# Optimization experiments

Hardware: AMD Instinct MI355X
Metric: run time of the kernel (lower is better)

## Reference

```python
import jax, jax.numpy as jnp
import numpy as np

DIM = 1024
DIM_HEAD = 64
HEADS = 8
INNER = DIM_HEAD * HEADS
EPS = 1e-5


def setup_inputs() -> dict:
    key = jax.random.key(0)
    ks = jax.random.split(key, 5)
    b, n = 4, 2048
    x = jax.random.normal(ks[0], (b, n, DIM), dtype=jnp.float32)
    mask = jnp.ones((b, n), dtype=bool)
    gamma = jnp.ones((DIM,), dtype=jnp.float32)
    null_kv = jax.random.normal(ks[1], (HEADS, 2, DIM_HEAD), dtype=jnp.float32)
    w_qkv = jax.random.normal(ks[2], (DIM, INNER * 3), dtype=jnp.float32) * (DIM ** -0.5)
    w_out = jax.random.normal(ks[3], (INNER, DIM), dtype=jnp.float32) * (INNER ** -0.5)
    return {"x": x, "mask": mask, "gamma": gamma, "null_kv": null_kv,
            "w_qkv": w_qkv, "w_out": w_out}


def _attention(x, mask, gamma, null_kv, w_qkv, w_out):
    b, n, _ = x.shape
    scale = DIM_HEAD ** -0.5
    # RMSNorm (sum-based, as in source): x * rsqrt(sum(x^2) + eps) * gamma * sqrt(dim)
    inv = jax.lax.rsqrt(jnp.sum(x * x, axis=-1, keepdims=True) + EPS)
    xn = x * inv * gamma * (DIM ** 0.5)
    qkv = xn @ w_qkv  # [b, n, 3*inner]
    q, k, v = jnp.split(qkv, 3, axis=-1)
    # b n (h d) -> b h n d
    to_heads = lambda t: t.reshape(b, n, HEADS, DIM_HEAD).transpose(0, 2, 1, 3)
    q, k, v = to_heads(q), to_heads(k), to_heads(v)
    # null kv token prepended along the key axis
    nk = jnp.broadcast_to(null_kv[:, 0][None, :, None, :], (b, HEADS, 1, DIM_HEAD))
    nv = jnp.broadcast_to(null_kv[:, 1][None, :, None, :], (b, HEADS, 1, DIM_HEAD))
    k = jnp.concatenate([nk, k], axis=2)  # [b, h, n+1, d]
    v = jnp.concatenate([nv, v], axis=2)
    q = q * scale
    sim = jnp.einsum('bhid,bhjd->bhij', q, k)  # [b, h, n, n+1]
    max_neg = -jnp.finfo(sim.dtype).max
    # padding mask, padded with True for the null token
    pad_mask = jnp.concatenate([jnp.ones((b, 1), dtype=bool), mask], axis=1)  # [b, n+1]
    sim = jnp.where(pad_mask[:, None, None, :], sim, max_neg)
    # causal mask over the non-null keys; null token (j=0) always visible
    j_idx = jnp.arange(n + 1)
    i_idx = jnp.arange(n)
    causal = (j_idx[None, :] - 1) > i_idx[:, None]  # True where masked
    sim = jnp.where(causal[None, None, :, :], max_neg, sim)
    attn = jax.nn.softmax(sim, axis=-1)
    out = jnp.einsum('bhij,bhjd->bhid', attn, v)  # [b, h, n, d]
    out = out.transpose(0, 2, 1, 3).reshape(b, n, INNER)
    return out @ w_out


def reference(x, mask, gamma, null_kv, w_qkv, w_out):
    return _attention(x, mask, gamma, null_kv, w_qkv, w_out)
```

## Files before the change

### kernel.cpp

```cpp
#include <hip/hip_runtime.h>

typedef unsigned short ushort_t;
typedef __attribute__((ext_vector_type(8))) unsigned short u16x8;
typedef __attribute__((ext_vector_type(4))) unsigned short u16x4;
typedef __attribute__((ext_vector_type(8))) __bf16 bf16x8;
typedef __attribute__((ext_vector_type(4))) float f32x4;

#define NB 4
#define NSEQ 2048
#define NH 8
#define DH 64
#define DMODEL 1024
#define INNERD 512

__device__ inline float b2f(unsigned short s) {
  union { unsigned u; float f; } v; v.u = ((unsigned)s) << 16; return v.f;
}
__device__ inline unsigned short f2b(float f) {
  unsigned u = __float_as_uint(f);
  u += 0x7fffu + ((u >> 16) & 1u);
  return (unsigned short)(u >> 16);
}
__device__ inline float fexp2(float x) {
  float r; asm("v_exp_f32 %0, %1" : "=v"(r) : "v"(x)); return r;
}
__device__ inline f32x4 mfma16(u16x8 a, u16x8 b, f32x4 c) {
  return __builtin_amdgcn_mfma_f32_16x16x32_bf16(
      __builtin_bit_cast(bf16x8, a), __builtin_bit_cast(bf16x8, b), c, 0, 0, 0);
}
__device__ inline void gload_lds16(const ushort_t* g, ushort_t* l) {
  __builtin_amdgcn_global_load_lds(
      (const __attribute__((address_space(1))) void*)g,
      (__attribute__((address_space(3))) void*)l, 16, 0, 0);
}

__global__ __launch_bounds__(256) void transconv_k(const float* __restrict__ in,
                                                   ushort_t* __restrict__ out,
                                                   int R, int C) {
  __shared__ float t[32][33];
  int c0 = blockIdx.x * 32, r0 = blockIdx.y * 32;
  int lx = threadIdx.x & 31, ly = threadIdx.x >> 5;
#pragma unroll
  for (int i = 0; i < 32; i += 8)
    t[ly + i][lx] = in[(size_t)(r0 + ly + i) * C + c0 + lx];
  __syncthreads();
#pragma unroll
  for (int i = 0; i < 32; i += 8)
    out[(size_t)(c0 + ly + i) * R + r0 + lx] = f2b(t[lx][ly + i]);
}

__global__ __launch_bounds__(256) void rmsnorm_k(const float* __restrict__ x,
                                                 const float* __restrict__ g,
                                                 ushort_t* __restrict__ xn) {
  int row = blockIdx.x, tid = threadIdx.x;
  const float* xr = x + (size_t)row * DMODEL;
  float4 v = *(const float4*)(xr + tid * 4);
  float f[4] = {v.x, v.y, v.z, v.w};
  float ss = f[0] * f[0] + f[1] * f[1] + f[2] * f[2] + f[3] * f[3];
#pragma unroll
  for (int d = 32; d; d >>= 1) ss += __shfl_xor(ss, d, 64);
  __shared__ float red[4];
  if ((tid & 63) == 0) red[tid >> 6] = ss;
  __syncthreads();
  float sum = red[0] + red[1] + red[2] + red[3];
  float inv = rsqrtf(sum + 1e-5f) * 32.0f;
  float4 gv = *(const float4*)(g + tid * 4);
  float gg[4] = {gv.x, gv.y, gv.z, gv.w};
  u16x4 o;
#pragma unroll
  for (int i = 0; i < 4; ++i) o[i] = f2b(f[i] * inv * gg[i]);
  *(u16x4*)(xn + (size_t)row * DMODEL + tid * 4) = o;
}

template <int OUT_F32>
__global__ __launch_bounds__(256) void gemm_k(const ushort_t* __restrict__ A,
                                              const ushort_t* __restrict__ Bt,
                                              void* __restrict__ Cv,
                                              int M, int Nn, int K) {
  __shared__ __align__(16) ushort_t As[128 * 64];
  __shared__ __align__(16) ushort_t Bs[128 * 64];
  int bn = blockIdx.x * 128, bm = blockIdx.y * 128;
  int tid = threadIdx.x;
  int w = tid >> 6, l = tid & 63, lg = l >> 4, lc = l & 15;
  int wm = (w >> 1) * 64, wn = (w & 1) * 64;
  f32x4 acc[4][4];
#pragma unroll
  for (int i = 0; i < 4; ++i)
#pragma unroll
    for (int j = 0; j < 4; ++j) acc[i][j] = (f32x4){0.f, 0.f, 0.f, 0.f};
  int rsub = l >> 3;
  int gsrc = ((l & 7) ^ rsub) * 8;
  for (int k0 = 0; k0 < K; k0 += 64) {
    __syncthreads();
#pragma unroll
    for (int i = 0; i < 4; ++i) {
      int rbase = w * 32 + i * 8;
      gload_lds16(&A[(size_t)(bm + rbase + rsub) * K + k0 + gsrc], &As[rbase * 64]);
      gload_lds16(&Bt[(size_t)(bn + rbase + rsub) * K + k0 + gsrc], &Bs[rbase * 64]);
    }
    __syncthreads();
#pragma unroll
    for (int kk = 0; kk < 2; ++kk) {
      u16x8 af[4], bfr[4];
#pragma unroll
      for (int i = 0; i < 4; ++i) {
        int ra = wm + i * 16 + lc;
        af[i] = *(const u16x8*)&As[ra * 64 + ((kk * 32 + lg * 8) ^ ((ra & 7) * 8))];
        int rb = wn + i * 16 + lc;
        bfr[i] = *(const u16x8*)&Bs[rb * 64 + ((kk * 32 + lg * 8) ^ ((rb & 7) * 8))];
      }
#pragma unroll
      for (int i = 0; i < 4; ++i)
#pragma unroll
        for (int j = 0; j < 4; ++j)
          acc[i][j] = mfma16(af[i], bfr[j], acc[i][j]);
    }
  }
#pragma unroll
  for (int i = 0; i < 4; ++i)
#pragma unroll
    for (int j = 0; j < 4; ++j) {
      int row = bm + wm + i * 16 + lg * 4;
      int col = bn + wn + j * 16 + lc;
#pragma unroll
      for (int e = 0; e < 4; ++e) {
        if (OUT_F32)
          ((float*)Cv)[(size_t)(row + e) * Nn + col] = acc[i][j][e];
        else
          ((ushort_t*)Cv)[(size_t)(row + e) * Nn + col] = f2b(acc[i][j][e]);
      }
    }
}

__global__ __launch_bounds__(256) void packkv_k(const ushort_t* __restrict__ qkv,
                                                ushort_t* __restrict__ kt,
                                                ushort_t* __restrict__ vtl) {
  int tt = blockIdx.x, bh = blockIdx.y;
  int b = bh >> 3, h = bh & 7;
  int u = threadIdx.x;
  int chunk = u >> 6, l = u & 63, lc = l & 15, lg = l >> 4;
  size_t tbase = ((size_t)bh * 64 + tt) * 2048;
  int f = chunk >> 1, kk = chunk & 1;
  *(u16x8*)&kt[tbase + u * 8] =
      *(const u16x8*)&qkv[(size_t)(b * NSEQ + tt * 32 + f * 16 + lc) * 1536 +
                          512 + h * 64 + kk * 32 + lg * 8];
  __shared__ __align__(16) ushort_t tv[32][72];
  int r = u >> 3, c8 = (u & 7) * 8;
  *(u16x8*)&tv[r][c8] =
      *(const u16x8*)&qkv[(size_t)(b * NSEQ + tt * 32 + r) * 1536 + 1024 + h * 64 + c8];
  __syncthreads();
  u16x8 o;
#pragma unroll
  for (int j = 0; j < 8; ++j) {
    int sig = lg * 4 + (j & 3) + ((j & 4) << 2);
    o[j] = tv[sig][chunk * 16 + lc];
  }
  *(u16x8*)&vtl[tbase + u * 8] = o;
}

__global__ __launch_bounds__(256) void attn_k(const ushort_t* __restrict__ qkv,
                                              const ushort_t* __restrict__ kt,
                                              const ushort_t* __restrict__ vtl,
                                              const float* __restrict__ nkv,
                                              ushort_t* __restrict__ aout) {
  int bid = blockIdx.x;
  int tid = threadIdx.x;
  int w = tid >> 6, l = tid & 63, lg = l >> 4, lc = l & 15;
  int s = 63 - (bid >> 5);
  int bh = ((bid & 7) << 2) | ((bid >> 3) & 3);
  int b = bh >> 3, h = bh & 7;
  int i0w = s * 32;

  __shared__ float Om[3][64][17];
  __shared__ float Ml[4][2][2][16];

  const float SCL2 = 0.18033688f;
  const float THR2 = 11.541561f;
  const float M2I = -1.0e30f;
  const float MSK = -3.0e38f;

  u16x8 q[2][2];
#pragma unroll
  for (int qi = 0; qi < 2; ++qi) {
    const ushort_t* qp =
        qkv + (size_t)(b * NSEQ + i0w + qi * 16 + lc) * 1536 + h * 64 + lg * 8;
    q[qi][0] = *(const u16x8*)(qp);
    q[qi][1] = *(const u16x8*)(qp + 32);
  }

  float m2[2], lsum[2];
  f32x4 O[2][4];
  if (w == 0) {
    float nd0 = 0.f, nd1 = 0.f;
#pragma unroll
    for (int kk = 0; kk < 2; ++kk) {
      const float* np = nkv + h * 128 + kk * 32 + lg * 8;
      float4 u = *(const float4*)(np);
      float4 vv = *(const float4*)(np + 4);
      float nk[8] = {u.x, u.y, u.z, u.w, vv.x, vv.y, vv.z, vv.w};
#pragma unroll
      for (int j = 0; j < 8; ++j) {
        nd0 += b2f(q[0][kk][j]) * nk[j];
        nd1 += b2f(q[1][kk][j]) * nk[j];
      }
    }
    nd0 += __shfl_xor(nd0, 16, 64); nd0 += __shfl_xor(nd0, 32, 64);
    nd1 += __shfl_xor(nd1, 16, 64); nd1 += __shfl_xor(nd1, 32, 64);
    m2[0] = nd0 * SCL2; m2[1] = nd1 * SCL2;
    lsum[0] = 0.25f; lsum[1] = 0.25f;
#pragma unroll
    for (int c = 0; c < 4; ++c) {
      float nv = nkv[h * 128 + 64 + c * 16 + lc];
      O[0][c] = (f32x4){nv, nv, nv, nv};
      O[1][c] = (f32x4){nv, nv, nv, nv};
    }
  } else {
    m2[0] = M2I; m2[1] = M2I;
    lsum[0] = 0.f; lsum[1] = 0.f;
#pragma unroll
    for (int c = 0; c < 4; ++c) {
      O[0][c] = (f32x4){0.f, 0.f, 0.f, 0.f};
      O[1][c] = (f32x4){0.f, 0.f, 0.f, 0.f};
    }
  }

  const ushort_t* ktb = kt + ((size_t)bh * 64) * 2048 + l * 8;
  const ushort_t* vtb = vtl + ((size_t)bh * 64) * 2048 + l * 8;

#define LOADK(dst, t_)                                                         \
  do {                                                                         \
    const ushort_t* kp = ktb + (size_t)(t_) * 2048;                            \
    dst[0][0] = *(const u16x8*)(kp);                                           \
    dst[0][1] = *(const u16x8*)(kp + 512);                                     \
    dst[1][0] = *(const u16x8*)(kp + 1024);                                    \
    dst[1][1] = *(const u16x8*)(kp + 1536);                                    \
  } while (0)
#define LOADV(dst, t_)                                                         \
  do {                                                                         \
    const ushort_t* vp = vtb + (size_t)(t_) * 2048;                            \
    dst[0] = *(const u16x8*)(vp);                                              \
    dst[1] = *(const u16x8*)(vp + 512);                                        \
    dst[2] = *(const u16x8*)(vp + 1024);                                       \
    dst[3] = *(const u16x8*)(vp + 1536);                                       \
  } while (0)

  auto body = [&](u16x8(&kf)[2][2], u16x8(&vb)[4], int t, bool last) {
    int k0 = t * 32;
    f32x4 sacc[2][2];
#pragma unroll
    for (int qi = 0; qi < 2; ++qi)
#pragma unroll
      for (int f = 0; f < 2; ++f) {
        sacc[qi][f] = mfma16(kf[f][0], q[qi][0], (f32x4){0.f, 0.f, 0.f, 0.f});
        sacc[qi][f] = mfma16(kf[f][1], q[qi][1], sacc[qi][f]);
      }
    float sv[2][2][4];
    float lmax[2];
#pragma unroll
    for (int qi = 0; qi < 2; ++qi) {
      int qrow = i0w + qi * 16 + lc;
#pragma unroll
      for (int f = 0; f < 2; ++f)
#pragma unroll
        for (int e = 0; e < 4; ++e) {
          float vvv = sacc[qi][f][e] * SCL2;
          if (last && (k0 + f * 16 + lg * 4 + e > qrow)) vvv = MSK;
          sv[qi][f][e] = vvv;
        }
      float a0 = fmaxf(sv[qi][0][0], sv[qi][0][1]);
      float a1 = fmaxf(sv[qi][0][2], sv[qi][0][3]);
      float a2 = fmaxf(sv[qi][1][0], sv[qi][1][1]);
      float a3 = fmaxf(sv[qi][1][2], sv[qi][1][3]);
      lmax[qi] = fmaxf(fmaxf(a0, a1), fmaxf(a2, a3));
    }
    bool need = (lmax[0] > m2[0] + THR2) || (lmax[1] > m2[1] + THR2);
    if (__any(need)) {
#pragma unroll
      for (int qi = 0; qi < 2; ++qi) {
        float mx = fmaxf(lmax[qi], __shfl_xor(lmax[qi], 16, 64));
        mx = fmaxf(mx, __shfl_xor(mx, 32, 64));
        float mn = fmaxf(m2[qi], mx);
        float al = fexp2(m2[qi] - mn);
        m2[qi] = mn;
        lsum[qi] *= al;
        float alr[4];
#pragma unroll
        for (int e = 0; e < 4; ++e) alr[e] = __shfl(al, lg * 4 + e, 64);
#pragma unroll
        for (int c = 0; c < 4; ++c)
#pragma unroll
          for (int e = 0; e < 4; ++e) O[qi][c][e] *= alr[e];
      }
    }
#pragma unroll
    for (int qi = 0; qi < 2; ++qi) {
      float pv[2][4];
#pragma unroll
      for (int f = 0; f < 2; ++f)
#pragma unroll
        for (int e = 0; e < 4; ++e)
          pv[f][e] = fexp2(sv[qi][f][e] - m2[qi]);
      float s0 = (pv[0][0] + pv[0][1]) + (pv[0][2] + pv[0][3]);
      float s1 = (pv[1][0] + pv[1][1]) + (pv[1][2] + pv[1][3]);
      lsum[qi] += s0 + s1;
      union { unsigned u[4]; u16x8 v8; } pa;
      asm("v_cvt_pk_bf16_f32 %0, %1, %2" : "=v"(pa.u[0]) : "v"(pv[0][0]), "v"(pv[0][1]));
      asm("v_cvt_pk_bf16_f32 %0, %1, %2" : "=v"(pa.u[1]) : "v"(pv[0][2]), "v"(pv[0][3]));
      asm("v_cvt_pk_bf16_f32 %0, %1, %2" : "=v"(pa.u[2]) : "v"(pv[1][0]), "v"(pv[1][1]));
      asm("v_cvt_pk_bf16_f32 %0, %1, %2" : "=v"(pa.u[3]) : "v"(pv[1][2]), "v"(pv[1][3]));
#pragma unroll
      for (int c = 0; c < 4; ++c) O[qi][c] = mfma16(pa.v8, vb[c], O[qi][c]);
    }
  };

  u16x8 kfA[2][2], kfB[2][2], vbA[4], vbB[4];
  int t = w;
  if (t <= s) {
    LOADK(kfA, t); LOADV(vbA, t);
    while (true) {
      bool more = (t + 4 <= s);
      if (more) { LOADK(kfB, t + 4); LOADV(vbB, t + 4); }
      body(kfA, vbA, t, t == s);
      if (!more) break;
      t += 4;
      more = (t + 4 <= s);
      if (more) { LOADK(kfA, t + 4); LOADV(vbA, t + 4); }
      body(kfB, vbB, t, t == s);
      if (!more) break;
      t += 4;
    }
  }
#undef LOADK
#undef LOADV

#pragma unroll
  for (int qi = 0; qi < 2; ++qi) {
    lsum[qi] += __shfl_xor(lsum[qi], 16, 64);
    lsum[qi] += __shfl_xor(lsum[qi], 32, 64);
  }
  if (l < 16) {
#pragma unroll
    for (int qi = 0; qi < 2; ++qi) {
      Ml[w][qi][0][lc] = m2[qi];
      Ml[w][qi][1][lc] = lsum[qi];
    }
  }
  for (int qi = 0; qi < 2; ++qi) {
    if (w > 0) {
#pragma unroll
      for (int c = 0; c < 4; ++c)
#pragma unroll
        for (int e = 0; e < 4; ++e) Om[w - 1][l][c * 4 + e] = O[qi][c][e];
    }
    __syncthreads();
    if (w == 0) {
#pragma unroll
      for (int e = 0; e < 4; ++e) {
        int r = lg * 4 + e;
        float mv0 = Ml[0][qi][0][r], mv1 = Ml[1][qi][0][r];
        float mv2 = Ml[2][qi][0][r], mv3 = Ml[3][qi][0][r];
        float mm = fmaxf(fmaxf(mv0, mv1), fmaxf(mv2, mv3));
        float e0 = fexp2(mv0 - mm), e1 = fexp2(mv1 - mm);
        float e2 = fexp2(mv2 - mm), e3 = fexp2(mv3 - mm);
        float ll = e0 * Ml[0][qi][1][r] + e1 * Ml[1][qi][1][r] +
                   e2 * Ml[2][qi][1][r] + e3 * Ml[3][qi][1][r];
        float rl = 1.0f / ll;
        int row = i0w + qi * 16 + r;
        size_t base = (size_t)(b * NSEQ + row) * INNERD + h * 64;
#pragma unroll
        for (int c = 0; c < 4; ++c) {
          int idx = c * 4 + e;
          float o = e0 * O[qi][c][e] + e1 * Om[0][l][idx] +
                    e2 * Om[1][l][idx] + e3 * Om[2][l][idx];
          aout[base + c * 16 + lc] = f2b(o * rl);
        }
      }
    }
    __syncthreads();
  }
}

extern "C" void kernel_launch(void* const* d_in, const int* in_sizes, int n_in,
                              void* d_out, int out_size, void* d_ws, size_t ws_size,
                              hipStream_t stream) {
  (void)in_sizes; (void)n_in; (void)out_size; (void)ws_size;
  const float* x    = (const float*)d_in[0];
  const float* g    = (const float*)d_in[2];
  const float* nkv  = (const float*)d_in[3];
  const float* wqkv = (const float*)d_in[4];
  const float* wout = (const float*)d_in[5];
  float* out = (float*)d_out;
  char* ws = (char*)d_ws;

  ushort_t* xn  = (ushort_t*)(ws);
  ushort_t* qkv = (ushort_t*)(ws + 16777216);
  ushort_t* kt  = (ushort_t*)(ws + 41943040);
  ushort_t* vtl = (ushort_t*)(ws + 50331648);
  ushort_t* wtq = (ushort_t*)(ws + 58720256);
  ushort_t* wto = (ushort_t*)(ws + 61865984);
  ushort_t* ao  = xn;

  transconv_k<<<dim3(1536 / 32, 1024 / 32), 256, 0, stream>>>(wqkv, wtq, 1024, 1536);
  transconv_k<<<dim3(1024 / 32, 512 / 32), 256, 0, stream>>>(wout, wto, 512, 1024);
  rmsnorm_k<<<8192, 256, 0, stream>>>(x, g, xn);
  gemm_k<0><<<dim3(12, 64), 256, 0, stream>>>(xn, wtq, qkv, 8192, 1536, 1024);
  packkv_k<<<dim3(64, 32), 256, 0, stream>>>(qkv, kt, vtl);
  attn_k<<<2048, 256, 0, stream>>>(qkv, kt, vtl, nkv, ao);
  gemm_k<1><<<dim3(8, 64), 256, 0, stream>>>(ao, wto, out, 8192, 1024, 512);
}
```

Baseline: 122.9 us.

## Fuse K/V packing into QKV GEMM epilogue and swizzle GEMM block order

The QKV GEMM epilogue now writes the K and V columns straight into the tiled layouts that attention consumes, so the separate packkv kernel and its extra read and write of K/V through global memory go away. Both GEMMs also switch to a 1D grid with a blockIdx remap that spreads consecutive blocks across eight groups, meant to improve cache locality or balance across XCDs. In exchange, the K/V epilogue writes are scattered 2-byte stores with heavier index arithmetic, which may coalesce poorly.

```diff
diff --git a/kernel.cpp b/kernel.cpp
--- a/kernel.cpp
+++ b/kernel.cpp
@@ -72,17 +72,22 @@
   *(u16x4*)(xn + (size_t)row * DMODEL + tid * 4) = o;
 }
 
-template <int OUT_F32>
+template <int MODE>
 __global__ __launch_bounds__(256) void gemm_k(const ushort_t* __restrict__ A,
                                               const ushort_t* __restrict__ Bt,
                                               void* __restrict__ Cv,
-                                              int M, int Nn, int K) {
-  __shared__ __align__(16) ushort_t As[128 * 64];
-  __shared__ __align__(16) ushort_t Bs[128 * 64];
-  int bn = blockIdx.x * 128, bm = blockIdx.y * 128;
+                                              void* __restrict__ Kp,
+                                              void* __restrict__ Vp,
+                                              int M, int Nn, int K, int cpx) {
+  int nbx = Nn >> 7;
+  int bid = blockIdx.x;
+  int swz = (bid & 7) * cpx + (bid >> 3);
+  int bn = (swz % nbx) * 128, bm = (swz / nbx) * 128;
   int tid = threadIdx.x;
   int w = tid >> 6, l = tid & 63, lg = l >> 4, lc = l & 15;
   int wm = (w >> 1) * 64, wn = (w & 1) * 64;
+  __shared__ __align__(16) ushort_t As[128 * 64];
+  __shared__ __align__(16) ushort_t Bs[128 * 64];
   f32x4 acc[4][4];
 #pragma unroll
   for (int i = 0; i < 4; ++i)
@@ -121,41 +126,50 @@
 #pragma unroll
     for (int j = 0; j < 4; ++j) {
       int row = bm + wm + i * 16 + lg * 4;
-      int col = bn + wn + j * 16 + lc;
-#pragma unroll
-      for (int e = 0; e < 4; ++e) {
-        if (OUT_F32)
+      int cb = bn + wn + j * 16;
+      int col = cb + lc;
+      if (MODE == 1) {
+#pragma unroll
+        for (int e = 0; e < 4; ++e)
           ((float*)Cv)[(size_t)(row + e) * Nn + col] = acc[i][j][e];
-        else
+      } else if (MODE == 0 || cb < 512) {
+#pragma unroll
+        for (int e = 0; e < 4; ++e)
           ((ushort_t*)Cv)[(size_t)(row + e) * Nn + col] = f2b(acc[i][j][e]);
-      }
-    }
-}
-
-__global__ __launch_bounds__(256) void packkv_k(const ushort_t* __restrict__ qkv,
-                                                ushort_t* __restrict__ kt,
-                                                ushort_t* __restrict__ vtl) {
-  int tt = blockIdx.x, bh = blockIdx.y;
-  int b = bh >> 3, h = bh & 7;
-  int u = threadIdx.x;
-  int chunk = u >> 6, l = u & 63, lc = l & 15, lg = l >> 4;
-  size_t tbase = ((size_t)bh * 64 + tt) * 2048;
-  int f = chunk >> 1, kk = chunk & 1;
-  *(u16x8*)&kt[tbase + u * 8] =
-      *(const u16x8*)&qkv[(size_t)(b * NSEQ + tt * 32 + f * 16 + lc) * 1536 +
-                          512 + h * 64 + kk * 32 + lg * 8];
-  __shared__ __align__(16) ushort_t tv[32][72];
-  int r = u >> 3, c8 = (u & 7) * 8;
-  *(u16x8*)&tv[r][c8] =
-      *(const u16x8*)&qkv[(size_t)(b * NSEQ + tt * 32 + r) * 1536 + 1024 + h * 64 + c8];
-  __syncthreads();
-  u16x8 o;
-#pragma unroll
-  for (int j = 0; j < 8; ++j) {
-    int sig = lg * 4 + (j & 3) + ((j & 4) << 2);
-    o[j] = tv[sig][chunk * 16 + lc];
-  }
-  *(u16x8*)&vtl[tbase + u * 8] = o;
+      } else if (cb < 1024) {
+        int h = (cb - 512) >> 6;
+        int d = (cb - 512) & 63;
+        d += lc;
+        int kk = d >> 5, dimgrp = (d >> 3) & 3, j2 = d & 7;
+        ushort_t* kt = (ushort_t*)Kp;
+#pragma unroll
+        for (int e = 0; e < 4; ++e) {
+          int n = row + e;
+          int b = n >> 11, nn2 = n & 2047;
+          int tt = nn2 >> 5, f = (nn2 >> 4) & 1, keylow = nn2 & 15;
+          size_t idx = (((size_t)(b * 8 + h) * 64 + tt) * 4 + f * 2 + kk) * 512 +
+                       (dimgrp * 16 + keylow) * 8 + j2;
+          kt[idx] = f2b(acc[i][j][e]);
+        }
+      } else {
+        int h = (cb - 1024) >> 6;
+        int d = (cb - 1024) & 63;
+        d += lc;
+        int chunk = d >> 4, lcV = d & 15;
+        ushort_t* vtl = (ushort_t*)Vp;
+#pragma unroll
+        for (int e = 0; e < 4; ++e) {
+          int n = row + e;
+          int b = n >> 11, nn2 = n & 2047;
+          int tt = nn2 >> 5, nn = nn2 & 31;
+          int j2 = (nn & 3) + ((nn >> 4) << 2);
+          int lgv = (nn >> 2) & 3;
+          size_t idx = (((size_t)(b * 8 + h) * 64 + tt) * 4 + chunk) * 512 +
+                       (lgv * 16 + lcV) * 8 + j2;
+          vtl[idx] = f2b(acc[i][j][e]);
+        }
+      }
+    }
 }
 
 __global__ __launch_bounds__(256) void attn_k(const ushort_t* __restrict__ qkv,
@@ -403,8 +417,7 @@
   transconv_k<<<dim3(1536 / 32, 1024 / 32), 256, 0, stream>>>(wqkv, wtq, 1024, 1536);
   transconv_k<<<dim3(1024 / 32, 512 / 32), 256, 0, stream>>>(wout, wto, 512, 1024);
   rmsnorm_k<<<8192, 256, 0, stream>>>(x, g, xn);
-  gemm_k<0><<<dim3(12, 64), 256, 0, stream>>>(xn, wtq, qkv, 8192, 1536, 1024);
-  packkv_k<<<dim3(64, 32), 256, 0, stream>>>(qkv, kt, vtl);
+  gemm_k<2><<<768, 256, 0, stream>>>(xn, wtq, qkv, kt, vtl, 8192, 1536, 1024, 96);
   attn_k<<<2048, 256, 0, stream>>>(qkv, kt, vtl, nkv, ao);
-  gemm_k<1><<<dim3(8, 64), 256, 0, stream>>>(ao, wto, out, 8192, 1024, 512);
-}
+  gemm_k<1><<<512, 256, 0, stream>>>(ao, wto, out, nullptr, nullptr, 8192, 1024, 512, 64);
+}
```

Result: faster. 112.5 us (-8.5%).
